# Optimization experiments

Hardware: AMD Instinct MI355X
Metric: run time of the kernel (lower is better)

Reference implementation:

```python
import jax, jax.numpy as jnp
import numpy as np

N = 51200      # total nodes
G = 256        # graphs in batch
NPG = 200      # nodes per graph
E = 409600     # intra-graph edges
EPG = E // G
F_IN, HID, HEADS, NCLS = 768, 128, 4, 2


def setup_inputs() -> dict:
    key = jax.random.key(0)
    ks = jax.random.split(key, 20)
    x = jax.random.normal(ks[0], (N, F_IN), jnp.float32)
    # edges strictly inside each graph, no self-loops (PyG batching semantics)
    gid = jnp.arange(E, dtype=jnp.int32) // EPG
    sl = jax.random.randint(ks[1], (E,), 0, NPG, dtype=jnp.int32)
    off = jax.random.randint(ks[2], (E,), 1, NPG, dtype=jnp.int32)
    dl = (sl + off) % NPG
    edge_index = jnp.stack([gid * NPG + sl, gid * NPG + dl])
    batch = jnp.arange(N, dtype=jnp.int32) // NPG

    def glorot(k, shape, fan_in):
        return jax.random.normal(k, shape, jnp.float32) * np.float32(1.0 / np.sqrt(fan_in))

    return {
        'x': x, 'edge_index': edge_index, 'batch': batch,
        'W1': glorot(ks[3], (F_IN, HEADS * HID), F_IN),
        'a_src1': glorot(ks[4], (HEADS, HID), HID),
        'a_dst1': glorot(ks[5], (HEADS, HID), HID),
        'b1': jnp.zeros((HEADS * HID,), jnp.float32),
        'W2': glorot(ks[6], (HEADS * HID, HID), HEADS * HID),
        'a_src2': glorot(ks[7], (1, HID), HID),
        'a_dst2': glorot(ks[8], (1, HID), HID),
        'b2': jnp.zeros((HID,), jnp.float32),
        'Wc': glorot(ks[9], (HID, 2), HID),
        'bc': jnp.zeros((2,), jnp.float32),
        'Wf1': glorot(ks[10], (HID, HID), HID),
        'bf1': jnp.zeros((HID,), jnp.float32),
        'Wf2': glorot(ks[11], (HID, NCLS), HID),
        'bf2': jnp.zeros((NCLS,), jnp.float32),
    }


def _segment_softmax(logits, seg, num):
    m = jax.ops.segment_max(logits, seg, num_segments=num)
    e = jnp.exp(logits - m[seg])
    s = jax.ops.segment_sum(e, seg, num_segments=num)
    return e / (s[seg] + 1e-16)


def _gat(x, src, dst, W, a_s, a_d, b, n):
    # PyG GATConv, eval mode (attention dropout off), self-loops already in src/dst
    H, C = a_s.shape
    h = (x @ W).reshape(n, H, C)                       # [n,H,C]
    a_src = (h * a_s).sum(-1)                          # [n,H]
    a_dst = (h * a_d).sum(-1)
    logits = jax.nn.leaky_relu(a_src[src] + a_dst[dst], 0.2)  # [Etot,H]
    alpha = _segment_softmax(logits, dst, n)
    out = jax.ops.segment_sum(h[src] * alpha[:, :, None], dst, num_segments=n)
    return out.reshape(n, H * C) + b


def reference(x, edge_index, batch, W1, a_src1, a_dst1, b1, W2, a_src2, a_dst2, b2,
              Wc, bc, Wf1, bf1, Wf2, bf2):
    src0, dst0 = edge_index[0], edge_index[1]
    loop = jnp.arange(N, dtype=src0.dtype)
    src = jnp.concatenate([src0, loop])
    dst = jnp.concatenate([dst0, loop])

    h1 = jax.nn.relu(_gat(x, src, dst, W1, a_src1, a_dst1, b1, N))     # [N,512]
    h2 = jax.nn.relu(_gat(h1, src, dst, W2, a_src2, a_dst2, b2, N))    # [N,128]

    S = jax.nn.softmax(h2 @ Wc + bc, axis=1)                           # [N,2]

    # aggregate(): per-graph S^T A S via per-edge outer products (A from original edges)
    eg = batch[src0]
    outer = S[src0][:, :, None] * S[dst0][:, None, :]                  # [E,2,2]
    agg = jax.ops.segment_sum(outer, eg, num_segments=G)               # [G,2,2]
    rnorm = jnp.clip(jnp.abs(agg).sum(axis=2, keepdims=True), 1e-5, None)  # F.normalize p=1 dim=1
    nadj = agg / rnorm
    diag = jnp.diagonal(nadj, axis1=1, axis2=2)                        # [G,2]
    aggregate_loss = jnp.mean(jnp.mean((diag - 1.0) ** 2, axis=1))     # MSE vs ones, averaged over graphs

    # subgraph embedding: first row of S_g^T x_g per graph
    sub = jax.ops.segment_sum(S[:, 0:1] * h2, batch, num_segments=G)   # [G,128]

    out = jax.nn.relu(sub @ Wf1 + bf1)                                 # eval: dropout off
    out = out @ Wf2 + bf2                                              # [G,2]
    return out, aggregate_loss
```

## Files before the change

kernel.cpp:

```cpp
#include <hip/hip_runtime.h>
#include <hip/hip_bf16.h>
#include <cstdint>

#define N_NODES 51200
#define N_GRAPH 256
#define NPG     200
#define N_EDGE  409600
#define EPG     1600
#define F_IN    768
#define HID     128
#define HEADS   4
#define HC      512

typedef __attribute__((ext_vector_type(8))) short short8;
typedef __attribute__((ext_vector_type(4))) float floatx4;

constexpr size_t OFF_H1B    = 0;
constexpr size_t OFF_H2B    = OFF_H1B + (size_t)N_NODES * HC * 2;
constexpr size_t OFF_H2F    = OFF_H2B + (size_t)N_NODES * HID * 2;
constexpr size_t OFF_WT1    = OFF_H2F + (size_t)N_NODES * HID * 4;
constexpr size_t OFF_WT2    = OFF_WT1 + (size_t)HC * F_IN * 2;
constexpr size_t OFF_S      = OFF_WT2 + (size_t)HID * HC * 2;
constexpr size_t OFF_AGG    = OFF_S + (size_t)N_NODES * 2 * 4;
constexpr size_t OFF_SUB    = OFF_AGG + (size_t)N_GRAPH * 4 * 4;

__device__ __forceinline__ float leaky(float x) { return x >= 0.0f ? x : 0.2f * x; }

__device__ __forceinline__ unsigned short f2bf(float f) {
    unsigned int u = __float_as_uint(f);
    u += 0x7fffu + ((u >> 16) & 1u);
    return (unsigned short)(u >> 16);
}
__device__ __forceinline__ float bflo(int p) { return __uint_as_float((unsigned)p << 16); }
__device__ __forceinline__ float bfhi(int p) { return __uint_as_float((unsigned)p & 0xffff0000u); }

__device__ __forceinline__ unsigned int cvtpk(float lo, float hi) {
    unsigned int r;
    asm("v_cvt_pk_bf16_f32 %0, %1, %2" : "=v"(r) : "v"(lo), "v"(hi));
    return r;
}

__device__ __forceinline__ void gl_lds16(const void* g, void* l) {
    __builtin_amdgcn_global_load_lds(
        (__attribute__((address_space(1))) void*)(g),
        (__attribute__((address_space(3))) void*)(l),
        16, 0, 0);
}

__global__ __launch_bounds__(256)
void transpose_cvt_kernel(const float* __restrict__ W, short* __restrict__ Wt,
                          int K, int Nn)
{
    int idx = blockIdx.x * 256 + threadIdx.x;
    if (idx >= K * Nn) return;
    int k = idx / Nn, n = idx % Nn;
    Wt[(size_t)n * K + k] = (short)f2bf(W[idx]);
}

__global__ __launch_bounds__(256, 3)
void gemm_xw1_kernel(const float* __restrict__ A, const short* __restrict__ Bt,
                     unsigned short* __restrict__ C, int M, int Nn, int K)
{
    __shared__ __align__(16) float Asm[2][128 * 32];
    __shared__ __align__(16) short Bsm[2][4096];
    const int tid = threadIdx.x;
    const int w = tid >> 6, l = tid & 63;

    const int nwg = gridDim.x;
    int wg = blockIdx.x;
    wg = (wg & 7) * (nwg >> 3) + (wg >> 3);
    const int nbx = Nn >> 7;
    const int m0 = (wg / nbx) * 128;
    const int n0 = (wg % nbx) * 128;
    const int wr = w >> 1, wc = w & 1;

    floatx4 acc[4][4];
#pragma unroll
    for (int i = 0; i < 4; ++i)
#pragma unroll
        for (int j = 0; j < 4; ++j) acc[i][j] = (floatx4)0.0f;

    const short* bgp = Bt + (size_t)(n0 + w * 32 + (l & 15)) * K + ((l >> 4) * 8);
    const float* agp = A + (size_t)(m0 + w * 32 + (l & 7)) * K + ((l >> 3) * 4);
    const int nt = K >> 5;

    int aB[4];
#pragma unroll
    for (int mi = 0; mi < 4; ++mi)
        aB[mi] = (wr * 8 + mi * 2 + ((l & 15) >> 3)) * 256 + (l >> 4) * 64 + (l & 7) * 4;
    const int bB0 = wc * 2048 + l * 8;

#define STAGE1(buf, t) {                                                        \
        const int ko_ = (t) * 32;                                               \
        gl_lds16(agp + ko_,              &Asm[buf][w * 1024]);                  \
        gl_lds16(agp + 8 * K + ko_,      &Asm[buf][w * 1024 + 256]);            \
        gl_lds16(agp + 16 * K + ko_,     &Asm[buf][w * 1024 + 512]);            \
        gl_lds16(agp + 24 * K + ko_,     &Asm[buf][w * 1024 + 768]);            \
        gl_lds16(bgp + ko_,              &Bsm[buf][w * 1024]);                  \
        gl_lds16(bgp + 16 * K + ko_,     &Bsm[buf][w * 1024 + 512]); }

#define COMPUTE1(buf) {                                                         \
        short8 af[4], bfr[4];                                                   \
        _Pragma("unroll")                                                       \
        for (int mi = 0; mi < 4; ++mi) {                                        \
            float4 v0 = *(const float4*)&Asm[buf][aB[mi]];                      \
            float4 v1 = *(const float4*)&Asm[buf][aB[mi] + 32];                 \
            uint4 pk;                                                           \
            pk.x = cvtpk(v0.x, v0.y); pk.y = cvtpk(v0.z, v0.w);                 \
            pk.z = cvtpk(v1.x, v1.y); pk.w = cvtpk(v1.z, v1.w);                 \
            af[mi] = *reinterpret_cast<short8*>(&pk);                           \
        }                                                                       \
        _Pragma("unroll")                                                       \
        for (int ni = 0; ni < 4; ++ni)                                          \
            bfr[ni] = *(const short8*)&Bsm[buf][bB0 + ni * 512];                \
        _Pragma("unroll")                                                       \
        for (int mi = 0; mi < 4; ++mi)                                          \
            _Pragma("unroll")                                                   \
            for (int ni = 0; ni < 4; ++ni)                                      \
                acc[mi][ni] = __builtin_amdgcn_mfma_f32_16x16x32_bf16(          \
                    af[mi], bfr[ni], acc[mi][ni], 0, 0, 0); }

    STAGE1(0, 0);
    asm volatile("s_waitcnt vmcnt(0)" ::: "memory");
    __builtin_amdgcn_s_barrier();

    int cur = 0;
    for (int t = 0; t < nt; ++t) {
        if (t + 1 < nt) STAGE1(cur ^ 1, t + 1);
        COMPUTE1(cur);
        if (t + 1 < nt) {
            asm volatile("s_waitcnt vmcnt(0) lgkmcnt(0)" ::: "memory");
            __builtin_amdgcn_s_barrier();
            cur ^= 1;
        }
    }
#undef STAGE1
#undef COMPUTE1

    const int lr = (l >> 4) * 4, lc = l & 15;
#pragma unroll
    for (int mi = 0; mi < 4; ++mi)
#pragma unroll
        for (int ni = 0; ni < 4; ++ni) {
            const size_t base = (size_t)(m0 + wr * 64 + mi * 16 + lr) * Nn
                              + (n0 + wc * 64 + ni * 16 + lc);
#pragma unroll
            for (int rr = 0; rr < 4; ++rr)
                C[base + (size_t)rr * Nn] = f2bf(acc[mi][ni][rr]);
        }
}

__global__ __launch_bounds__(256, 3)
void gemm_bf16_kernel(const short* __restrict__ Ab, const short* __restrict__ Bt,
                      unsigned short* __restrict__ C, int M, int Nn, int K)
{
    __shared__ __align__(16) short Bblob[3][4096];
    __shared__ __align__(16) short Ablob[3][4096];
    const int tid = threadIdx.x;
    const int w = tid >> 6, l = tid & 63;

    const int nwg = gridDim.x;
    int wg = blockIdx.x;
    wg = (wg & 7) * (nwg >> 3) + (wg >> 3);
    const int nbx = Nn >> 7;
    const int m0 = (wg / nbx) * 128;
    const int n0 = (wg % nbx) * 128;
    const int wr = w >> 1, wc = w & 1;
    const int wofs = w * 1024;

    floatx4 acc[4][4];
#pragma unroll
    for (int i = 0; i < 4; ++i)
#pragma unroll
        for (int j = 0; j < 4; ++j) acc[i][j] = (floatx4)0.0f;

    const short* bgp = Bt + (size_t)(n0 + w * 32 + (l & 15)) * K + ((l >> 4) * 8);
    const short* agp = Ab + (size_t)(m0 + w * 32 + (l & 15)) * K + ((l >> 4) * 8);
    const int nt = K >> 5;

    auto compute = [&](int bi) {
        short8 af[4], bfr[4];
#pragma unroll
        for (int mi = 0; mi < 4; ++mi)
            af[mi] = *(const short8*)&Ablob[bi][(wr * 4 + mi) * 512 + l * 8];
#pragma unroll
        for (int ni = 0; ni < 4; ++ni)
            bfr[ni] = *(const short8*)&Bblob[bi][(wc * 4 + ni) * 512 + l * 8];
#pragma unroll
        for (int mi = 0; mi < 4; ++mi)
#pragma unroll
            for (int ni = 0; ni < 4; ++ni)
                acc[mi][ni] = __builtin_amdgcn_mfma_f32_16x16x32_bf16(
                    af[mi], bfr[ni], acc[mi][ni], 0, 0, 0);
    };

    gl_lds16(agp,               &Ablob[0][wofs]);
    gl_lds16(agp + 16 * K,      &Ablob[0][wofs + 512]);
    gl_lds16(bgp,               &Bblob[0][wofs]);
    gl_lds16(bgp + 16 * K,      &Bblob[0][wofs + 512]);
    gl_lds16(agp + 32,          &Ablob[1][wofs]);
    gl_lds16(agp + 16 * K + 32, &Ablob[1][wofs + 512]);
    gl_lds16(bgp + 32,          &Bblob[1][wofs]);
    gl_lds16(bgp + 16 * K + 32, &Bblob[1][wofs + 512]);
    asm volatile("s_waitcnt vmcnt(4)" ::: "memory");
    __builtin_amdgcn_s_barrier();

    int cur3 = 0;
    for (int t = 0; t < nt; ++t) {
        int nn3 = cur3 + 2; if (nn3 >= 3) nn3 -= 3;
        if (t + 2 < nt) {
            const int kk = (t + 2) << 5;
            gl_lds16(agp + kk,          &Ablob[nn3][wofs]);
            gl_lds16(agp + 16 * K + kk, &Ablob[nn3][wofs + 512]);
            gl_lds16(bgp + kk,          &Bblob[nn3][wofs]);
            gl_lds16(bgp + 16 * K + kk, &Bblob[nn3][wofs + 512]);
        }
        compute(cur3);
        if (t + 1 < nt) {
            if (t + 2 < nt) asm volatile("s_waitcnt vmcnt(4) lgkmcnt(0)" ::: "memory");
            else            asm volatile("s_waitcnt vmcnt(0) lgkmcnt(0)" ::: "memory");
            __builtin_amdgcn_s_barrier();
        }
        cur3 += 1; if (cur3 == 3) cur3 = 0;
    }

    const int lr = (l >> 4) * 4, lc = l & 15;
#pragma unroll
    for (int mi = 0; mi < 4; ++mi)
#pragma unroll
        for (int ni = 0; ni < 4; ++ni) {
            const size_t base = (size_t)(m0 + wr * 64 + mi * 16 + lr) * Nn
                              + (n0 + wc * 64 + ni * 16 + lc);
#pragma unroll
            for (int rr = 0; rr < 4; ++rr)
                C[base + (size_t)rr * Nn] = f2bf(acc[mi][ni][rr]);
        }
}

__global__ __launch_bounds__(512)
void gat1_kernel(const unsigned short* __restrict__ H, const int* __restrict__ src0,
                 const int* __restrict__ dst0, const float* __restrict__ a_s,
                 const float* __restrict__ a_d, const float* __restrict__ b1,
                 unsigned short* __restrict__ out)
{
    const int g = blockIdx.x, h = blockIdx.y;
    __shared__ int   s_feat[NPG * 64];
    __shared__ float s_as[NPG], s_ad[NPG], s_m[NPG], s_inv[NPG];
    __shared__ int   s_row[NPG + 1];
    __shared__ int   s_cnt[NPG];
    __shared__ int   s_scan[256];
    __shared__ unsigned short s_eraw[EPG];
    __shared__ int2  s_wc[EPG];
    const int tid = threadIdx.x, w = tid >> 6, l = tid & 63;
    const int gbase = g * NPG;

    for (int flat = tid; flat < NPG * 16; flat += 512) {
        int row = flat >> 4, q = flat & 15;
        uint4 v = *(const uint4*)(H + (size_t)(gbase + row) * HC + h * HID + q * 8);
        *(uint4*)&s_feat[row * 64 + q * 4] = v;
    }
    for (int j = tid; j < EPG; j += 512) {
        int s = src0[g * EPG + j] - gbase;
        int d = dst0[g * EPG + j] - gbase;
        s_eraw[j] = (unsigned short)(s | (d << 8));
    }
    if (tid < NPG) s_cnt[tid] = 0;
    __syncthreads();

    for (int j = tid; j < EPG; j += 512)
        atomicAdd(&s_cnt[s_eraw[j] >> 8], 1);
    const float2 av = ((const float2*)(a_s + h * HID))[l];
    const float2 dv = ((const float2*)(a_d + h * HID))[l];
    for (int nl = w; nl < NPG; nl += 8) {
        int pk = s_feat[nl * 64 + l];
        float f0 = bflo(pk), f1 = bfhi(pk);
        float ss = f0 * av.x + f1 * av.y;
        float sd = f0 * dv.x + f1 * dv.y;
#pragma unroll
        for (int off = 1; off < 64; off <<= 1) {
            ss += __shfl_xor(ss, off);
            sd += __shfl_xor(sd, off);
        }
        if (l == 0) { s_as[nl] = ss; s_ad[nl] = sd; }
    }
    __syncthreads();

    {
        int v = (tid < NPG) ? s_cnt[tid] : 0;
        if (tid < 256) s_scan[tid] = v;
        __syncthreads();
        for (int off = 1; off < 256; off <<= 1) {
            int u = (tid >= off && tid < 256) ? s_scan[tid - off] : 0;
            __syncthreads();
            if (tid < 256) s_scan[tid] += u;
            __syncthreads();
        }
        if (tid < NPG) s_row[tid + 1] = s_scan[tid];
        if (tid == 0) s_row[0] = 0;
        __syncthreads();
        if (tid < NPG) s_scan[tid] = s_row[tid];
    }
    __syncthreads();

    for (int j = tid; j < EPG; j += 512) {
        int pk = s_eraw[j];
        int p = atomicAdd(&s_scan[pk >> 8], 1);
        s_wc[p].y = pk;
    }
    __syncthreads();

    for (int j = tid; j < EPG; j += 512) {
        int pk = s_wc[j].y;
        s_wc[j].x = __float_as_int(leaky(s_as[pk & 255] + s_ad[pk >> 8]));
    }
    __syncthreads();

    if (tid < NPG) {
        float m = leaky(s_as[tid] + s_ad[tid]);
        int r0 = s_row[tid], r1 = s_row[tid + 1];
        for (int j = r0; j < r1; ++j) m = fmaxf(m, __int_as_float(s_wc[j].x));
        s_m[tid] = m;
    }
    __syncthreads();

    for (int j = tid; j < EPG; j += 512) {
        int2 e = s_wc[j];
        s_wc[j].x = __float_as_int(__expf(__int_as_float(e.x) - s_m[e.y >> 8]));
    }
    __syncthreads();

    if (tid < NPG) {
        float rs = __expf(leaky(s_as[tid] + s_ad[tid]) - s_m[tid]);
        int r0 = s_row[tid], r1 = s_row[tid + 1];
        for (int j = r0; j < r1; ++j) rs += __int_as_float(s_wc[j].x);
        s_inv[tid] = 1.0f / (rs + 1e-16f);
    }
    __syncthreads();

    const float2 bv = ((const float2*)(b1 + h * HID))[l];
    for (int nl = w; nl < NPG; nl += 8) {
        const int r0 = s_row[nl], r1 = s_row[nl + 1];
        const float wself = __expf(leaky(s_as[nl] + s_ad[nl]) - s_m[nl]);
        int spk = s_feat[nl * 64 + l];
        float a0 = wself * bflo(spk), a1 = wself * bfhi(spk);
        float c0 = 0.0f, c1 = 0.0f;
        int j = r0;
        for (; j + 4 <= r1; j += 4) {
            int2 e0 = s_wc[j], e1 = s_wc[j + 1], e2 = s_wc[j + 2], e3 = s_wc[j + 3];
            int p0 = s_feat[(e0.y & 255) * 64 + l];
            int p1 = s_feat[(e1.y & 255) * 64 + l];
            int p2 = s_feat[(e2.y & 255) * 64 + l];
            int p3 = s_feat[(e3.y & 255) * 64 + l];
            float w0 = __int_as_float(e0.x), w1 = __int_as_float(e1.x);
            float w2 = __int_as_float(e2.x), w3 = __int_as_float(e3.x);
            a0 += w0 * bflo(p0); a1 += w0 * bfhi(p0);
            c0 += w1 * bflo(p1); c1 += w1 * bfhi(p1);
            a0 += w2 * bflo(p2); a1 += w2 * bfhi(p2);
            c0 += w3 * bflo(p3); c1 += w3 * bfhi(p3);
        }
        for (; j < r1; ++j) {
            int2 e0 = s_wc[j];
            int p0 = s_feat[(e0.y & 255) * 64 + l];
            float w0 = __int_as_float(e0.x);
            a0 += w0 * bflo(p0); a1 += w0 * bfhi(p0);
        }
        const float inv = s_inv[nl];
        float o0 = (a0 + c0) * inv + bv.x;
        float o1 = (a1 + c1) * inv + bv.y;
        unsigned int st = (unsigned int)f2bf(fmaxf(o0, 0.0f))
                        | ((unsigned int)f2bf(fmaxf(o1, 0.0f)) << 16);
        *(unsigned int*)&out[(size_t)(gbase + nl) * HC + h * HID + 2 * l] = st;
    }
}

__global__ __launch_bounds__(512)
void gat2_kernel(const unsigned short* __restrict__ H, const int* __restrict__ src0,
                 const int* __restrict__ dst0, const float* __restrict__ a_s,
                 const float* __restrict__ a_d, const float* __restrict__ b2,
                 const float* __restrict__ Wc, const float* __restrict__ bc,
                 float* __restrict__ sub, float* __restrict__ agg)
{
    const int g = blockIdx.x;
    __shared__ int   s_feat[NPG * 64];
    __shared__ float s_as[NPG], s_ad[NPG], s_m[NPG], s_inv[NPG];
    __shared__ int   s_row[NPG + 1];
    __shared__ int   s_cnt[NPG];
    __shared__ int   s_scan[256];
    __shared__ unsigned short s_eraw[EPG];
    __shared__ int2  s_wc[EPG];
    __shared__ float2 s_Sv[NPG];
    __shared__ float  s_red[8 * 128];
    __shared__ float  s_aggr[8][4];
    const int tid = threadIdx.x, w = tid >> 6, l = tid & 63;
    const int gbase = g * NPG;

    for (int flat = tid; flat < NPG * 16; flat += 512) {
        int row = flat >> 4, q = flat & 15;
        uint4 v = *(const uint4*)(H + (size_t)(gbase + row) * HID + q * 8);
        *(uint4*)&s_feat[row * 64 + q * 4] = v;
    }
    for (int j = tid; j < EPG; j += 512) {
        int s = src0[g * EPG + j] - gbase;
        int d = dst0[g * EPG + j] - gbase;
        s_eraw[j] = (unsigned short)(s | (d << 8));
    }
    if (tid < NPG) s_cnt[tid] = 0;
    __syncthreads();

    for (int j = tid; j < EPG; j += 512)
        atomicAdd(&s_cnt[s_eraw[j] >> 8], 1);
    const float2 av = ((const float2*)a_s)[l];
    const float2 dv = ((const float2*)a_d)[l];
    for (int nl = w; nl < NPG; nl += 8) {
        int pk = s_feat[nl * 64 + l];
        float f0 = bflo(pk), f1 = bfhi(pk);
        float ss = f0 * av.x + f1 * av.y;
        float sd = f0 * dv.x + f1 * dv.y;
#pragma unroll
        for (int off = 1; off < 64; off <<= 1) {
            ss += __shfl_xor(ss, off);
            sd += __shfl_xor(sd, off);
        }
        if (l == 0) { s_as[nl] = ss; s_ad[nl] = sd; }
    }
    __syncthreads();

    {
        int v = (tid < NPG) ? s_cnt[tid] : 0;
        if (tid < 256) s_scan[tid] = v;
        __syncthreads();
        for (int off = 1; off < 256; off <<= 1) {
            int u = (tid >= off && tid < 256) ? s_scan[tid - off] : 0;
            __syncthreads();
            if (tid < 256) s_scan[tid] += u;
            __syncthreads();
        }
        if (tid < NPG) s_row[tid + 1] = s_scan[tid];
        if (tid == 0) s_row[0] = 0;
        __syncthreads();
        if (tid < NPG) s_scan[tid] = s_row[tid];
    }
    __syncthreads();

    for (int j = tid; j < EPG; j += 512) {
        int pk = s_eraw[j];
        int p = atomicAdd(&s_scan[pk >> 8], 1);
        s_wc[p].y = pk;
    }
    __syncthreads();

    for (int j = tid; j < EPG; j += 512) {
        int pk = s_wc[j].y;
        s_wc[j].x = __float_as_int(leaky(s_as[pk & 255] + s_ad[pk >> 8]));
    }
    __syncthreads();

    if (tid < NPG) {
        float m = leaky(s_as[tid] + s_ad[tid]);
        int r0 = s_row[tid], r1 = s_row[tid + 1];
        for (int j = r0; j < r1; ++j) m = fmaxf(m, __int_as_float(s_wc[j].x));
        s_m[tid] = m;
    }
    __syncthreads();

    for (int j = tid; j < EPG; j += 512) {
        int2 e = s_wc[j];
        s_wc[j].x = __float_as_int(__expf(__int_as_float(e.x) - s_m[e.y >> 8]));
    }
    __syncthreads();

    if (tid < NPG) {
        float rs = __expf(leaky(s_as[tid] + s_ad[tid]) - s_m[tid]);
        int r0 = s_row[tid], r1 = s_row[tid + 1];
        for (int j = r0; j < r1; ++j) rs += __int_as_float(s_wc[j].x);
        s_inv[tid] = 1.0f / (rs + 1e-16f);
    }
    __syncthreads();

    const float2 bv = ((const float2*)b2)[l];
    const float4 wcv = ((const float4*)Wc)[l];
    const float bc0 = bc[0], bc1 = bc[1];
    float accs0 = 0.0f, accs1 = 0.0f;
    for (int nl = w; nl < NPG; nl += 8) {
        const int r0 = s_row[nl], r1 = s_row[nl + 1];
        const float wself = __expf(leaky(s_as[nl] + s_ad[nl]) - s_m[nl]);
        int spk = s_feat[nl * 64 + l];
        float a0 = wself * bflo(spk), a1 = wself * bfhi(spk);
        float c0 = 0.0f, c1 = 0.0f;
        int j = r0;
        for (; j + 4 <= r1; j += 4) {
            int2 e0 = s_wc[j], e1 = s_wc[j + 1], e2 = s_wc[j + 2], e3 = s_wc[j + 3];
            int p0 = s_feat[(e0.y & 255) * 64 + l];
            int p1 = s_feat[(e1.y & 255) * 64 + l];
            int p2 = s_feat[(e2.y & 255) * 64 + l];
            int p3 = s_feat[(e3.y & 255) * 64 + l];
            float w0 = __int_as_float(e0.x), w1 = __int_as_float(e1.x);
            float w2 = __int_as_float(e2.x), w3 = __int_as_float(e3.x);
            a0 += w0 * bflo(p0); a1 += w0 * bfhi(p0);
            c0 += w1 * bflo(p1); c1 += w1 * bfhi(p1);
            a0 += w2 * bflo(p2); a1 += w2 * bfhi(p2);
            c0 += w3 * bflo(p3); c1 += w3 * bfhi(p3);
        }
        for (; j < r1; ++j) {
            int2 e0 = s_wc[j];
            int p0 = s_feat[(e0.y & 255) * 64 + l];
            float w0 = __int_as_float(e0.x);
            a0 += w0 * bflo(p0); a1 += w0 * bfhi(p0);
        }
        const float inv = s_inv[nl];
        float o0 = fmaxf((a0 + c0) * inv + bv.x, 0.0f);
        float o1 = fmaxf((a1 + c1) * inv + bv.y, 0.0f);
        float z0 = o0 * wcv.x + o1 * wcv.z;
        float z1 = o0 * wcv.y + o1 * wcv.w;
#pragma unroll
        for (int off = 1; off < 64; off <<= 1) {
            z0 += __shfl_xor(z0, off);
            z1 += __shfl_xor(z1, off);
        }
        z0 += bc0; z1 += bc1;
        float mm = fmaxf(z0, z1);
        float e0 = __expf(z0 - mm), e1 = __expf(z1 - mm);
        float is = 1.0f / (e0 + e1);
        float s0v = e0 * is, s1v = e1 * is;
        if (l == 0) s_Sv[nl] = make_float2(s0v, s1v);
        accs0 += s0v * o0;
        accs1 += s0v * o1;
    }
    s_red[w * 128 + 2 * l]     = accs0;
    s_red[w * 128 + 2 * l + 1] = accs1;
    __syncthreads();

    float a00 = 0, a01 = 0, a10 = 0, a11 = 0;
    for (int j = tid; j < EPG; j += 512) {
        int pk = s_eraw[j];
        float2 Ss = s_Sv[pk & 255];
        float2 Sd = s_Sv[pk >> 8];
        a00 += Ss.x * Sd.x; a01 += Ss.x * Sd.y;
        a10 += Ss.y * Sd.x; a11 += Ss.y * Sd.y;
    }
#pragma unroll
    for (int off = 32; off > 0; off >>= 1) {
        a00 += __shfl_down(a00, off); a01 += __shfl_down(a01, off);
        a10 += __shfl_down(a10, off); a11 += __shfl_down(a11, off);
    }
    if (l == 0) { s_aggr[w][0] = a00; s_aggr[w][1] = a01; s_aggr[w][2] = a10; s_aggr[w][3] = a11; }
    __syncthreads();

    if (tid < 128) {
        float s = 0.0f;
#pragma unroll
        for (int w8 = 0; w8 < 8; ++w8) s += s_red[w8 * 128 + tid];
        sub[(size_t)g * HID + tid] = s;
    }
    if (tid < 4) {
        float s = 0.0f;
#pragma unroll
        for (int w8 = 0; w8 < 8; ++w8) s += s_aggr[w8][tid];
        agg[g * 4 + tid] = s;
    }
}

__global__ __launch_bounds__(256)
void loss_kernel(const float* __restrict__ agg, float* __restrict__ out_loss)
{
    int tid = threadIdx.x;
    float a00 = agg[tid*4 + 0], a01 = agg[tid*4 + 1];
    float a10 = agg[tid*4 + 2], a11 = agg[tid*4 + 3];
    float rn0 = fmaxf(fabsf(a00) + fabsf(a01), 1e-5f);
    float rn1 = fmaxf(fabsf(a10) + fabsf(a11), 1e-5f);
    float d0 = a00 / rn0 - 1.0f, d1 = a11 / rn1 - 1.0f;
    float contrib = 0.5f * (d0*d0 + d1*d1);
    for (int off = 32; off > 0; off >>= 1) contrib += __shfl_down(contrib, off);
    __shared__ float sred[4];
    if ((tid & 63) == 0) sred[tid >> 6] = contrib;
    __syncthreads();
    if (tid == 0)
        out_loss[0] = (sred[0] + sred[1] + sred[2] + sred[3]) * (1.0f / N_GRAPH);
}

__global__ __launch_bounds__(128)
void final_kernel(const float* __restrict__ sub, const float* __restrict__ Wf1,
                  const float* __restrict__ bf1, const float* __restrict__ Wf2,
                  const float* __restrict__ bf2, float* __restrict__ out)
{
    __shared__ float s_sub[128];
    __shared__ float s_fc[128];
    const int g = blockIdx.x, t = threadIdx.x;
    s_sub[t] = sub[g*HID + t];
    __syncthreads();
    float acc = bf1[t];
    for (int c = 0; c < 128; ++c)
        acc += s_sub[c] * Wf1[c*128 + t];
    s_fc[t] = fmaxf(acc, 0.0f);
    __syncthreads();
    if (t < 2) {
        float z = bf2[t];
        for (int j = 0; j < 128; ++j) z += s_fc[j] * Wf2[j*2 + t];
        out[g*2 + t] = z;
    }
}

extern "C" void kernel_launch(void* const* d_in, const int* in_sizes, int n_in,
                              void* d_out, int out_size, void* d_ws, size_t ws_size,
                              hipStream_t stream)
{
    const float* x   = (const float*)d_in[0];
    const int*   ei  = (const int*)d_in[1];
    const float* W1  = (const float*)d_in[3];
    const float* as1 = (const float*)d_in[4];
    const float* ad1 = (const float*)d_in[5];
    const float* b1  = (const float*)d_in[6];
    const float* W2  = (const float*)d_in[7];
    const float* as2 = (const float*)d_in[8];
    const float* ad2 = (const float*)d_in[9];
    const float* b2  = (const float*)d_in[10];
    const float* Wc  = (const float*)d_in[11];
    const float* bc  = (const float*)d_in[12];
    const float* Wf1 = (const float*)d_in[13];
    const float* bf1 = (const float*)d_in[14];
    const float* Wf2 = (const float*)d_in[15];
    const float* bf2 = (const float*)d_in[16];
    const int* src0 = ei;
    const int* dst0 = ei + N_EDGE;

    char* ws = (char*)d_ws;
    unsigned short* H1b = (unsigned short*)(ws + OFF_H1B);
    unsigned short* H2b = (unsigned short*)(ws + OFF_H2B);
    short* Wt1   = (short*)(ws + OFF_WT1);
    short* Wt2   = (short*)(ws + OFF_WT2);
    float* aggb  = (float*)(ws + OFF_AGG);
    float* subb  = (float*)(ws + OFF_SUB);
    float* out   = (float*)d_out;

    transpose_cvt_kernel<<<(F_IN*HC + 255)/256, 256, 0, stream>>>(W1, Wt1, F_IN, HC);
    transpose_cvt_kernel<<<(HC*HID + 255)/256, 256, 0, stream>>>(W2, Wt2, HC, HID);

    gemm_xw1_kernel<<<(N_NODES/128) * (HC/128), 256, 0, stream>>>(
        x, Wt1, H1b, N_NODES, HC, F_IN);

    gat1_kernel<<<dim3(N_GRAPH, HEADS), 512, 0, stream>>>(
        H1b, src0, dst0, as1, ad1, b1, H1b);

    gemm_bf16_kernel<<<(N_NODES/128) * (HID/128), 256, 0, stream>>>(
        (const short*)H1b, Wt2, H2b, N_NODES, HID, HC);

    gat2_kernel<<<N_GRAPH, 512, 0, stream>>>(
        H2b, src0, dst0, as2, ad2, b2, Wc, bc, subb, aggb);

    loss_kernel<<<1, 256, 0, stream>>>(aggb, out + N_GRAPH*2);
    final_kernel<<<N_GRAPH, 128, 0, stream>>>(subb, Wf1, bf1, Wf2, bf2, out);

    (void)in_sizes; (void)n_in; (void)out_size; (void)ws_size;
}
```

Measured before the change: 510.4 us.

## Halve GEMM M-tiles, simplify pipelining, and build edge CSR once for both GAT layers

Both GEMM kernels drop from 128-row to 64-row tiles, doubling the grid and raising the occupancy hint from 3 to 4 waves per SIMD. The bf16 GEMM's 3-stage prefetch becomes a simpler double buffer with full __syncthreads. A new csr_kernel sorts each graph's edges by destination once and stores the order and row offsets, so gat1 (run per head) and gat2 no longer redo the count, scan and scatter themselves. Smaller tiles reload the B operand more often and the shallower pipeline may hide less memory latency, in exchange for more parallel workgroups.

```diff
diff --git a/kernel.cpp b/kernel.cpp
--- a/kernel.cpp
+++ b/kernel.cpp
@@ -23,6 +23,8 @@
 constexpr size_t OFF_S      = OFF_WT2 + (size_t)HID * HC * 2;
 constexpr size_t OFF_AGG    = OFF_S + (size_t)N_NODES * 2 * 4;
 constexpr size_t OFF_SUB    = OFF_AGG + (size_t)N_GRAPH * 4 * 4;
+constexpr size_t OFF_EORD   = OFF_SUB + (size_t)N_GRAPH * HID * 4;
+constexpr size_t OFF_ROWS   = OFF_EORD + (size_t)N_GRAPH * EPG * 2;
 
 __device__ __forceinline__ float leaky(float x) { return x >= 0.0f ? x : 0.2f * x; }
 
@@ -57,11 +59,11 @@
     Wt[(size_t)n * K + k] = (short)f2bf(W[idx]);
 }
 
-__global__ __launch_bounds__(256, 3)
+__global__ __launch_bounds__(256, 4)
 void gemm_xw1_kernel(const float* __restrict__ A, const short* __restrict__ Bt,
                      unsigned short* __restrict__ C, int M, int Nn, int K)
 {
-    __shared__ __align__(16) float Asm[2][128 * 32];
+    __shared__ __align__(16) float Asm[2][64 * 32];
     __shared__ __align__(16) short Bsm[2][4096];
     const int tid = threadIdx.x;
     const int w = tid >> 6, l = tid & 63;
@@ -70,39 +72,39 @@
     int wg = blockIdx.x;
     wg = (wg & 7) * (nwg >> 3) + (wg >> 3);
     const int nbx = Nn >> 7;
-    const int m0 = (wg / nbx) * 128;
+    const int m0 = (wg / nbx) * 64;
     const int n0 = (wg % nbx) * 128;
     const int wr = w >> 1, wc = w & 1;
 
-    floatx4 acc[4][4];
-#pragma unroll
-    for (int i = 0; i < 4; ++i)
+    floatx4 acc[2][4];
+#pragma unroll
+    for (int i = 0; i < 2; ++i)
 #pragma unroll
         for (int j = 0; j < 4; ++j) acc[i][j] = (floatx4)0.0f;
 
     const short* bgp = Bt + (size_t)(n0 + w * 32 + (l & 15)) * K + ((l >> 4) * 8);
-    const float* agp = A + (size_t)(m0 + w * 32 + (l & 7)) * K + ((l >> 3) * 4);
+    const float* agp = A + (size_t)(m0 + w * 16 + (l & 7)) * K + ((l >> 3) * 4);
     const int nt = K >> 5;
 
-    int aB[4];
-#pragma unroll
-    for (int mi = 0; mi < 4; ++mi)
-        aB[mi] = (wr * 8 + mi * 2 + ((l & 15) >> 3)) * 256 + (l >> 4) * 64 + (l & 7) * 4;
+    int aB[2];
+#pragma unroll
+    for (int mi = 0; mi < 2; ++mi) {
+        const int r = wr * 32 + mi * 16 + (l & 15);
+        aB[mi] = (r >> 3) * 256 + ((l >> 4) * 8 >> 2) * 32 + (r & 7) * 4;
+    }
     const int bB0 = wc * 2048 + l * 8;
 
 #define STAGE1(buf, t) {                                                        \
         const int ko_ = (t) * 32;                                               \
-        gl_lds16(agp + ko_,              &Asm[buf][w * 1024]);                  \
-        gl_lds16(agp + 8 * K + ko_,      &Asm[buf][w * 1024 + 256]);            \
-        gl_lds16(agp + 16 * K + ko_,     &Asm[buf][w * 1024 + 512]);            \
-        gl_lds16(agp + 24 * K + ko_,     &Asm[buf][w * 1024 + 768]);            \
+        gl_lds16(agp + ko_,              &Asm[buf][w * 512]);                   \
+        gl_lds16(agp + 8 * K + ko_,      &Asm[buf][w * 512 + 256]);             \
         gl_lds16(bgp + ko_,              &Bsm[buf][w * 1024]);                  \
         gl_lds16(bgp + 16 * K + ko_,     &Bsm[buf][w * 1024 + 512]); }
 
 #define COMPUTE1(buf) {                                                         \
-        short8 af[4], bfr[4];                                                   \
+        short8 af[2], bfr[4];                                                   \
         _Pragma("unroll")                                                       \
-        for (int mi = 0; mi < 4; ++mi) {                                        \
+        for (int mi = 0; mi < 2; ++mi) {                                        \
             float4 v0 = *(const float4*)&Asm[buf][aB[mi]];                      \
             float4 v1 = *(const float4*)&Asm[buf][aB[mi] + 32];                 \
             uint4 pk;                                                           \
@@ -114,35 +116,31 @@
         for (int ni = 0; ni < 4; ++ni)                                          \
             bfr[ni] = *(const short8*)&Bsm[buf][bB0 + ni * 512];                \
         _Pragma("unroll")                                                       \
-        for (int mi = 0; mi < 4; ++mi)                                          \
+        for (int mi = 0; mi < 2; ++mi)                                          \
             _Pragma("unroll")                                                   \
             for (int ni = 0; ni < 4; ++ni)                                      \
                 acc[mi][ni] = __builtin_amdgcn_mfma_f32_16x16x32_bf16(          \
                     af[mi], bfr[ni], acc[mi][ni], 0, 0, 0); }
 
     STAGE1(0, 0);
-    asm volatile("s_waitcnt vmcnt(0)" ::: "memory");
-    __builtin_amdgcn_s_barrier();
+    __syncthreads();
 
     int cur = 0;
     for (int t = 0; t < nt; ++t) {
         if (t + 1 < nt) STAGE1(cur ^ 1, t + 1);
         COMPUTE1(cur);
-        if (t + 1 < nt) {
-            asm volatile("s_waitcnt vmcnt(0) lgkmcnt(0)" ::: "memory");
-            __builtin_amdgcn_s_barrier();
-            cur ^= 1;
-        }
+        __syncthreads();
+        cur ^= 1;
     }
 #undef STAGE1
 #undef COMPUTE1
 
     const int lr = (l >> 4) * 4, lc = l & 15;
 #pragma unroll
-    for (int mi = 0; mi < 4; ++mi)
+    for (int mi = 0; mi < 2; ++mi)
 #pragma unroll
         for (int ni = 0; ni < 4; ++ni) {
-            const size_t base = (size_t)(m0 + wr * 64 + mi * 16 + lr) * Nn
+            const size_t base = (size_t)(m0 + wr * 32 + mi * 16 + lr) * Nn
                               + (n0 + wc * 64 + ni * 16 + lc);
 #pragma unroll
             for (int rr = 0; rr < 4; ++rr)
@@ -150,12 +148,12 @@
         }
 }
 
-__global__ __launch_bounds__(256, 3)
+__global__ __launch_bounds__(256, 4)
 void gemm_bf16_kernel(const short* __restrict__ Ab, const short* __restrict__ Bt,
                       unsigned short* __restrict__ C, int M, int Nn, int K)
 {
-    __shared__ __align__(16) short Bblob[3][4096];
-    __shared__ __align__(16) short Ablob[3][4096];
+    __shared__ __align__(16) short Asm[2][2048];
+    __shared__ __align__(16) short Bsm[2][4096];
     const int tid = threadIdx.x;
     const int w = tid >> 6, l = tid & 63;
 
@@ -163,73 +161,62 @@
     int wg = blockIdx.x;
     wg = (wg & 7) * (nwg >> 3) + (wg >> 3);
     const int nbx = Nn >> 7;
-    const int m0 = (wg / nbx) * 128;
+    const int m0 = (wg / nbx) * 64;
     const int n0 = (wg % nbx) * 128;
     const int wr = w >> 1, wc = w & 1;
-    const int wofs = w * 1024;
-
-    floatx4 acc[4][4];
-#pragma unroll
-    for (int i = 0; i < 4; ++i)
+
+    floatx4 acc[2][4];
+#pragma unroll
+    for (int i = 0; i < 2; ++i)
 #pragma unroll
         for (int j = 0; j < 4; ++j) acc[i][j] = (floatx4)0.0f;
 
     const short* bgp = Bt + (size_t)(n0 + w * 32 + (l & 15)) * K + ((l >> 4) * 8);
-    const short* agp = Ab + (size_t)(m0 + w * 32 + (l & 15)) * K + ((l >> 4) * 8);
+    const short* agp = Ab + (size_t)(m0 + w * 16 + (l & 15)) * K + ((l >> 4) * 8);
     const int nt = K >> 5;
 
-    auto compute = [&](int bi) {
-        short8 af[4], bfr[4];
-#pragma unroll
-        for (int mi = 0; mi < 4; ++mi)
-            af[mi] = *(const short8*)&Ablob[bi][(wr * 4 + mi) * 512 + l * 8];
-#pragma unroll
-        for (int ni = 0; ni < 4; ++ni)
-            bfr[ni] = *(const short8*)&Bblob[bi][(wc * 4 + ni) * 512 + l * 8];
-#pragma unroll
-        for (int mi = 0; mi < 4; ++mi)
-#pragma unroll
-            for (int ni = 0; ni < 4; ++ni)
-                acc[mi][ni] = __builtin_amdgcn_mfma_f32_16x16x32_bf16(
-                    af[mi], bfr[ni], acc[mi][ni], 0, 0, 0);
-    };
-
-    gl_lds16(agp,               &Ablob[0][wofs]);
-    gl_lds16(agp + 16 * K,      &Ablob[0][wofs + 512]);
-    gl_lds16(bgp,               &Bblob[0][wofs]);
-    gl_lds16(bgp + 16 * K,      &Bblob[0][wofs + 512]);
-    gl_lds16(agp + 32,          &Ablob[1][wofs]);
-    gl_lds16(agp + 16 * K + 32, &Ablob[1][wofs + 512]);
-    gl_lds16(bgp + 32,          &Bblob[1][wofs]);
-    gl_lds16(bgp + 16 * K + 32, &Bblob[1][wofs + 512]);
-    asm volatile("s_waitcnt vmcnt(4)" ::: "memory");
-    __builtin_amdgcn_s_barrier();
-
-    int cur3 = 0;
+    const int bB0 = wc * 2048 + l * 8;
+
+#define STAGE2(buf, t) {                                                        \
+        const int ko_ = (t) * 32;                                               \
+        gl_lds16(agp + ko_,              &Asm[buf][w * 512]);                   \
+        gl_lds16(bgp + ko_,              &Bsm[buf][w * 1024]);                  \
+        gl_lds16(bgp + 16 * K + ko_,     &Bsm[buf][w * 1024 + 512]); }
+
+#define COMPUTE2(buf) {                                                         \
+        short8 af[2], bfr[4];                                                   \
+        _Pragma("unroll")                                                       \
+        for (int mi = 0; mi < 2; ++mi)                                          \
+            af[mi] = *(const short8*)&Asm[buf][(wr * 2 + mi) * 512 + l * 8];    \
+        _Pragma("unroll")                                                       \
+        for (int ni = 0; ni < 4; ++ni)                                          \
+            bfr[ni] = *(const short8*)&Bsm[buf][bB0 + ni * 512];                \
+        _Pragma("unroll")                                                       \
+        for (int mi = 0; mi < 2; ++mi)                                          \
+            _Pragma("unroll")                                                   \
+            for (int ni = 0; ni < 4; ++ni)                                      \
+                acc[mi][ni] = __builtin_amdgcn_mfma_f32_16x16x32_bf16(          \
+                    af[mi], bfr[ni], acc[mi][ni], 0, 0, 0); }
+
+    STAGE2(0, 0);
+    __syncthreads();
+
+    int cur = 0;
     for (int t = 0; t < nt; ++t) {
-        int nn3 = cur3 + 2; if (nn3 >= 3) nn3 -= 3;
-        if (t + 2 < nt) {
-            const int kk = (t + 2) << 5;
-            gl_lds16(agp + kk,          &Ablob[nn3][wofs]);
-            gl_lds16(agp + 16 * K + kk, &Ablob[nn3][wofs + 512]);
-            gl_lds16(bgp + kk,          &Bblob[nn3][wofs]);
-            gl_lds16(bgp + 16 * K + kk, &Bblob[nn3][wofs + 512]);
-        }
-        compute(cur3);
-        if (t + 1 < nt) {
-            if (t + 2 < nt) asm volatile("s_waitcnt vmcnt(4) lgkmcnt(0)" ::: "memory");
-            else            asm volatile("s_waitcnt vmcnt(0) lgkmcnt(0)" ::: "memory");
-            __builtin_amdgcn_s_barrier();
-        }
-        cur3 += 1; if (cur3 == 3) cur3 = 0;
-    }
+        if (t + 1 < nt) STAGE2(cur ^ 1, t + 1);
+        COMPUTE2(cur);
+        __syncthreads();
+        cur ^= 1;
+    }
+#undef STAGE2
+#undef COMPUTE2
 
     const int lr = (l >> 4) * 4, lc = l & 15;
 #pragma unroll
-    for (int mi = 0; mi < 4; ++mi)
+    for (int mi = 0; mi < 2; ++mi)
 #pragma unroll
         for (int ni = 0; ni < 4; ++ni) {
-            const size_t base = (size_t)(m0 + wr * 64 + mi * 16 + lr) * Nn
+            const size_t base = (size_t)(m0 + wr * 32 + mi * 16 + lr) * Nn
                               + (n0 + wc * 64 + ni * 16 + lc);
 #pragma unroll
             for (int rr = 0; rr < 4; ++rr)
@@ -237,19 +224,61 @@
         }
 }
 
+__global__ __launch_bounds__(256)
+void csr_kernel(const int* __restrict__ src0, const int* __restrict__ dst0,
+                unsigned short* __restrict__ eord, int* __restrict__ rows)
+{
+    const int g = blockIdx.x, tid = threadIdx.x;
+    __shared__ unsigned short s_eraw[EPG];
+    __shared__ int s_cnt[NPG];
+    __shared__ int s_scan[256];
+    __shared__ int s_row[NPG + 1];
+    const int gbase = g * NPG;
+
+    if (tid < NPG) s_cnt[tid] = 0;
+    for (int j = tid; j < EPG; j += 256) {
+        int s = src0[g * EPG + j] - gbase;
+        int d = dst0[g * EPG + j] - gbase;
+        s_eraw[j] = (unsigned short)(s | (d << 8));
+    }
+    __syncthreads();
+    for (int j = tid; j < EPG; j += 256)
+        atomicAdd(&s_cnt[s_eraw[j] >> 8], 1);
+    __syncthreads();
+    {
+        int v = (tid < NPG) ? s_cnt[tid] : 0;
+        s_scan[tid] = v;
+        __syncthreads();
+        for (int off = 1; off < 256; off <<= 1) {
+            int u = (tid >= off) ? s_scan[tid - off] : 0;
+            __syncthreads();
+            s_scan[tid] += u;
+            __syncthreads();
+        }
+        if (tid < NPG) s_row[tid + 1] = s_scan[tid];
+        if (tid == 0) s_row[0] = 0;
+        __syncthreads();
+        if (tid < NPG) s_scan[tid] = s_row[tid];
+    }
+    __syncthreads();
+    for (int j = tid; j < EPG; j += 256) {
+        int pk = s_eraw[j];
+        int p = atomicAdd(&s_scan[pk >> 8], 1);
+        eord[(size_t)g * EPG + p] = (unsigned short)pk;
+    }
+    if (tid <= NPG) rows[g * (NPG + 1) + tid] = s_row[tid];
+}
+
 __global__ __launch_bounds__(512)
-void gat1_kernel(const unsigned short* __restrict__ H, const int* __restrict__ src0,
-                 const int* __restrict__ dst0, const float* __restrict__ a_s,
-                 const float* __restrict__ a_d, const float* __restrict__ b1,
-                 unsigned short* __restrict__ out)
+void gat1_kernel(const unsigned short* __restrict__ H,
+                 const unsigned short* __restrict__ eord, const int* __restrict__ rows,
+                 const float* __restrict__ a_s, const float* __restrict__ a_d,
+                 const float* __restrict__ b1, unsigned short* __restrict__ out)
 {
     const int g = blockIdx.x, h = blockIdx.y;
     __shared__ int   s_feat[NPG * 64];
     __shared__ float s_as[NPG], s_ad[NPG], s_m[NPG], s_inv[NPG];
     __shared__ int   s_row[NPG + 1];
-    __shared__ int   s_cnt[NPG];
-    __shared__ int   s_scan[256];
-    __shared__ unsigned short s_eraw[EPG];
     __shared__ int2  s_wc[EPG];
     const int tid = threadIdx.x, w = tid >> 6, l = tid & 63;
     const int gbase = g * NPG;
@@ -259,16 +288,11 @@
         uint4 v = *(const uint4*)(H + (size_t)(gbase + row) * HC + h * HID + q * 8);
         *(uint4*)&s_feat[row * 64 + q * 4] = v;
     }
-    for (int j = tid; j < EPG; j += 512) {
-        int s = src0[g * EPG + j] - gbase;
-        int d = dst0[g * EPG + j] - gbase;
-        s_eraw[j] = (unsigned short)(s | (d << 8));
-    }
-    if (tid < NPG) s_cnt[tid] = 0;
-    __syncthreads();
-
     for (int j = tid; j < EPG; j += 512)
-        atomicAdd(&s_cnt[s_eraw[j] >> 8], 1);
+        s_wc[j].y = eord[(size_t)g * EPG + j];
+    if (tid <= NPG) s_row[tid] = rows[g * (NPG + 1) + tid];
+    __syncthreads();
+
     const float2 av = ((const float2*)(a_s + h * HID))[l];
     const float2 dv = ((const float2*)(a_d + h * HID))[l];
     for (int nl = w; nl < NPG; nl += 8) {
@@ -282,30 +306,6 @@
             sd += __shfl_xor(sd, off);
         }
         if (l == 0) { s_as[nl] = ss; s_ad[nl] = sd; }
-    }
-    __syncthreads();
-
-    {
-        int v = (tid < NPG) ? s_cnt[tid] : 0;
-        if (tid < 256) s_scan[tid] = v;
-        __syncthreads();
-        for (int off = 1; off < 256; off <<= 1) {
-            int u = (tid >= off && tid < 256) ? s_scan[tid - off] : 0;
-            __syncthreads();
-            if (tid < 256) s_scan[tid] += u;
-            __syncthreads();
-        }
-        if (tid < NPG) s_row[tid + 1] = s_scan[tid];
-        if (tid == 0) s_row[0] = 0;
-        __syncthreads();
-        if (tid < NPG) s_scan[tid] = s_row[tid];
-    }
-    __syncthreads();
-
-    for (int j = tid; j < EPG; j += 512) {
-        int pk = s_eraw[j];
-        int p = atomicAdd(&s_scan[pk >> 8], 1);
-        s_wc[p].y = pk;
     }
     __syncthreads();
 
@@ -374,19 +374,17 @@
 }
 
 __global__ __launch_bounds__(512)
-void gat2_kernel(const unsigned short* __restrict__ H, const int* __restrict__ src0,
-                 const int* __restrict__ dst0, const float* __restrict__ a_s,
-                 const float* __restrict__ a_d, const float* __restrict__ b2,
-                 const float* __restrict__ Wc, const float* __restrict__ bc,
+void gat2_kernel(const unsigned short* __restrict__ H,
+                 const unsigned short* __restrict__ eord, const int* __restrict__ rows,
+                 const float* __restrict__ a_s, const float* __restrict__ a_d,
+                 const float* __restrict__ b2, const float* __restrict__ Wc,
+                 const float* __restrict__ bc,
                  float* __restrict__ sub, float* __restrict__ agg)
 {
     const int g = blockIdx.x;
     __shared__ int   s_feat[NPG * 64];
     __shared__ float s_as[NPG], s_ad[NPG], s_m[NPG], s_inv[NPG];
     __shared__ int   s_row[NPG + 1];
-    __shared__ int   s_cnt[NPG];
-    __shared__ int   s_scan[256];
-    __shared__ unsigned short s_eraw[EPG];
     __shared__ int2  s_wc[EPG];
     __shared__ float2 s_Sv[NPG];
     __shared__ float  s_red[8 * 128];
@@ -399,16 +397,11 @@
         uint4 v = *(const uint4*)(H + (size_t)(gbase + row) * HID + q * 8);
         *(uint4*)&s_feat[row * 64 + q * 4] = v;
     }
-    for (int j = tid; j < EPG; j += 512) {
-        int s = src0[g * EPG + j] - gbase;
-        int d = dst0[g * EPG + j] - gbase;
-        s_eraw[j] = (unsigned short)(s | (d << 8));
-    }
-    if (tid < NPG) s_cnt[tid] = 0;
-    __syncthreads();
-
     for (int j = tid; j < EPG; j += 512)
-        atomicAdd(&s_cnt[s_eraw[j] >> 8], 1);
+        s_wc[j].y = eord[(size_t)g * EPG + j];
+    if (tid <= NPG) s_row[tid] = rows[g * (NPG + 1) + tid];
+    __syncthreads();
+
     const float2 av = ((const float2*)a_s)[l];
     const float2 dv = ((const float2*)a_d)[l];
     for (int nl = w; nl < NPG; nl += 8) {
@@ -422,30 +415,6 @@
             sd += __shfl_xor(sd, off);
         }
         if (l == 0) { s_as[nl] = ss; s_ad[nl] = sd; }
-    }
-    __syncthreads();
-
-    {
-        int v = (tid < NPG) ? s_cnt[tid] : 0;
-        if (tid < 256) s_scan[tid] = v;
-        __syncthreads();
-        for (int off = 1; off < 256; off <<= 1) {
-            int u = (tid >= off && tid < 256) ? s_scan[tid - off] : 0;
-            __syncthreads();
-            if (tid < 256) s_scan[tid] += u;
-            __syncthreads();
-        }
-        if (tid < NPG) s_row[tid + 1] = s_scan[tid];
-        if (tid == 0) s_row[0] = 0;
-        __syncthreads();
-        if (tid < NPG) s_scan[tid] = s_row[tid];
-    }
-    __syncthreads();
-
-    for (int j = tid; j < EPG; j += 512) {
-        int pk = s_eraw[j];
-        int p = atomicAdd(&s_scan[pk >> 8], 1);
-        s_wc[p].y = pk;
     }
     __syncthreads();
 
@@ -532,7 +501,7 @@
 
     float a00 = 0, a01 = 0, a10 = 0, a11 = 0;
     for (int j = tid; j < EPG; j += 512) {
-        int pk = s_eraw[j];
+        int pk = s_wc[j].y;
         float2 Ss = s_Sv[pk & 255];
         float2 Sd = s_Sv[pk >> 8];
         a00 += Ss.x * Sd.x; a01 += Ss.x * Sd.y;
@@ -630,22 +599,25 @@
     short* Wt2   = (short*)(ws + OFF_WT2);
     float* aggb  = (float*)(ws + OFF_AGG);
     float* subb  = (float*)(ws + OFF_SUB);
+    unsigned short* eord = (unsigned short*)(ws + OFF_EORD);
+    int*   rowsb = (int*)(ws + OFF_ROWS);
     float* out   = (float*)d_out;
 
     transpose_cvt_kernel<<<(F_IN*HC + 255)/256, 256, 0, stream>>>(W1, Wt1, F_IN, HC);
     transpose_cvt_kernel<<<(HC*HID + 255)/256, 256, 0, stream>>>(W2, Wt2, HC, HID);
-
-    gemm_xw1_kernel<<<(N_NODES/128) * (HC/128), 256, 0, stream>>>(
+    csr_kernel<<<N_GRAPH, 256, 0, stream>>>(src0, dst0, eord, rowsb);
+
+    gemm_xw1_kernel<<<(N_NODES/64) * (HC/128), 256, 0, stream>>>(
         x, Wt1, H1b, N_NODES, HC, F_IN);
 
     gat1_kernel<<<dim3(N_GRAPH, HEADS), 512, 0, stream>>>(
-        H1b, src0, dst0, as1, ad1, b1, H1b);
-
-    gemm_bf16_kernel<<<(N_NODES/128) * (HID/128), 256, 0, stream>>>(
+        H1b, eord, rowsb, as1, ad1, b1, H1b);
+
+    gemm_bf16_kernel<<<(N_NODES/64) * (HID/128), 256, 0, stream>>>(
         (const short*)H1b, Wt2, H2b, N_NODES, HID, HC);
 
     gat2_kernel<<<N_GRAPH, 512, 0, stream>>>(
-        H2b, src0, dst0, as2, ad2, b2, Wc, bc, subb, aggb);
+        H2b, eord, rowsb, as2, ad2, b2, Wc, bc, subb, aggb);
 
     loss_kernel<<<1, 256, 0, stream>>>(aggb, out + N_GRAPH*2);
     final_kernel<<<N_GRAPH, 128, 0, stream>>>(subb, Wf1, bf1, Wf2, bf2, out);
```

Result: slower. 538.1 us (+5.4%).
